# Kernel tuning notes

Hardware: AMD Instinct MI355X
Metric: run time of the kernel (lower is better)

## Reference

```python
import jax, jax.numpy as jnp
import numpy as np

ALPHA = 0.1          # LeakyReLU negative slope
NEG = -9.0e15        # mask fill value (matches torch source)
S_OUT = 64           # source_out_features
T_OUT = 64           # target_out_features


def setup_inputs() -> dict:
    key = jax.random.key(0)
    ks = jax.random.split(key, 8)
    n_s, n_t = 8192, 4096
    s_in, t_in = 128, 128
    hs = jax.random.normal(ks[0], (n_s, s_in), dtype=jnp.float32)
    ht = jax.random.normal(ks[1], (n_t, t_in), dtype=jnp.float32)
    A_opt = jax.random.randint(ks[2], (n_t, n_s), 0, 2, dtype=jnp.int32)
    # xavier_uniform with gain=1.414
    def xavier(k, shape, gain=1.414):
        fan_in, fan_out = shape[0], shape[1]
        bound = gain * np.sqrt(6.0 / (fan_in + fan_out))
        return jax.random.uniform(k, shape, jnp.float32, -bound, bound)
    Ws = xavier(ks[3], (s_in, T_OUT))
    Wt = xavier(ks[4], (t_in, S_OUT))
    a1 = xavier(ks[5], (S_OUT + T_OUT, 1))
    bias_s = jnp.zeros((T_OUT,), jnp.float32)
    bias_t = jnp.zeros((S_OUT,), jnp.float32)
    return {"hs": hs, "ht": ht, "A_opt": A_opt, "Ws": Ws, "Wt": Wt,
            "a1": a1, "bias_s": bias_s, "bias_t": bias_t}


def reference(hs, ht, A_opt, Ws, Wt, a1, bias_s, bias_t):
    # Asymmetric HOAN, eval mode (dropout=0), concatenate=True.
    Whs = hs @ Ws                       # [n_s, t_out]
    Wht = ht @ Wt                       # [n_t, s_out]
    # a1 split: first S_OUT rows pair with Wht, remaining T_OUT rows with Whs
    a_t = a1[:S_OUT, :]                 # [s_out, 1]
    a_s = a1[S_OUT:, :]                 # [t_out, 1]
    Whst = Whs @ a_s                    # [n_s, 1]
    Whtt = Wht @ a_t                    # [n_t, 1]
    e_st = jax.nn.leaky_relu(Whtt + Whst.T, ALPHA)   # [n_t, n_s]
    e_ts = jax.nn.leaky_relu(Whst + Whtt.T, ALPHA)   # [n_s, n_t]
    mask = A_opt > 0                    # [n_t, n_s]
    att_st = jax.nn.softmax(jnp.where(mask, e_st, NEG), axis=1)
    h_prime_st = att_st @ Whs + bias_s  # [n_t, t_out]
    att_ts = jax.nn.softmax(jnp.where(mask.T, e_ts, NEG), axis=1)
    h_prime_ts = att_ts @ Wht + bias_t  # [n_s, s_out]
    return jax.nn.elu(h_prime_st), jax.nn.elu(h_prime_ts)
```

## Files before the change

### kernel.cpp

```cpp
#include <hip/hip_runtime.h>
#include <math.h>

#define N_S 8192
#define N_T 4096
#define DIN 128
#define NF  64
#define SPL0 8
#define SPL1 4

typedef __attribute__((ext_vector_type(8))) short short8;
typedef __attribute__((ext_vector_type(4))) float f32x4;
typedef __attribute__((ext_vector_type(4))) int i32x4;
typedef unsigned long long u64;
typedef unsigned int u32;

__device__ __forceinline__ unsigned short f2bf(float x){
  unsigned u = __float_as_uint(x);
  unsigned r = (u + 0x7fffu + ((u >> 16) & 1u)) >> 16;
  return (unsigned short)r;
}

__device__ __forceinline__ size_t xt2_idx(int f, int k){
  return ((size_t)(k >> 5))*2048 + (size_t)((f >> 4)*512 + ((k >> 3) & 3)*128 + (f & 15)*8 + (k & 7));
}

__global__ __launch_bounds__(256) void k1_fused(
    const int* __restrict__ A,
    u64* __restrict__ RBt,
    const float* __restrict__ hs, const float* __restrict__ ht,
    const float* __restrict__ Ws, const float* __restrict__ Wt,
    const float* __restrict__ a1,
    unsigned short* __restrict__ XT2s, unsigned short* __restrict__ XT2t,
    float* __restrict__ EFs, float* __restrict__ EFt)
{
  __shared__ __align__(16) float smem[DIN*NF + 4*DIN];
  int bx = blockIdx.x;
  int t = threadIdx.x;
  if (bx < 2048) {
    u64* rbS = (u64*)smem;
    int w = t >> 6, l = t & 63;
    int i = 2*bx + (w >> 1);
    int h = w & 1;
    const int* base = A + (size_t)i*N_S + h*4096;
    #pragma unroll
    for (int it = 0; it < 16; ++it) {
      i32x4 v = *(const i32x4*)(base + it*256 + 4*l);
      u32 nib = (v.x > 0 ? 1u : 0u) | (v.y > 0 ? 2u : 0u)
              | (v.z > 0 ? 4u : 0u) | (v.w > 0 ? 8u : 0u);
      u32 b8  = nib | (((u32)__shfl_xor((int)nib, 1, 64)) << 4);
      u32 b16 = b8  | (((u32)__shfl_xor((int)b8,  2, 64)) << 8);
      u32 b32 = b16 | (((u32)__shfl_xor((int)b16, 4, 64)) << 16);
      u32 hi  = (u32)__shfl_xor((int)b32, 8, 64);
      if ((l & 15) == 0)
        rbS[(size_t)(w>>1)*128 + h*64 + it*4 + (l>>4)] = (u64)b32 | ((u64)hi << 32);
    }
    __syncthreads();
    int wi = t >> 1, ri = t & 1;
    RBt[(size_t)wi*N_T + 2*bx + ri] = rbS[(size_t)ri*128 + wi];
  } else {
    int b = bx - 2048;
    float* Wl = smem;
    float* hrow = smem + DIN*NF;
    bool is_s = b < (N_S/4);
    const float* h; const float* W; const float* av;
    unsigned short* XT; float* EFd; int r0;
    if (is_s) { r0 = b*4;           h = hs; W = Ws; av = a1 + 64; XT = XT2s; EFd = EFs; }
    else      { r0 = (b - N_S/4)*4; h = ht; W = Wt; av = a1;      XT = XT2t; EFd = EFt; }
    for (int i = t; i < DIN*NF; i += 256) Wl[i] = W[i];
    for (int i = t; i < 4*DIN;  i += 256) hrow[i] = h[(size_t)r0*DIN + i];
    __syncthreads();
    int f = t & 63, sr = t >> 6;
    float acc = 0.f;
    #pragma unroll 8
    for (int k = 0; k < DIN; ++k) acc += hrow[sr*DIN + k] * Wl[k*NF + f];
    int r = r0 + sr;
    XT[xt2_idx(f, r)] = f2bf(acc);
    float p = acc * av[f];
    #pragma unroll
    for (int o = 32; o > 0; o >>= 1) p += __shfl_xor(p, o, 64);
    if (f == 0) { EFd[2*r] = __expf(p); EFd[2*r + 1] = __expf(0.1f*p); }
  }
}

template<int DIR>
__device__ __forceinline__ void agg_body(
    int rb, int split,
    const u64* __restrict__ RBt,
    const float* __restrict__ EFu, const float* __restrict__ EFk,
    const unsigned short* __restrict__ XT2,
    float* __restrict__ accP,
    float* __restrict__ sumP,
    u64* cbS)
{
  constexpr int NK = (DIR == 0) ? N_S : N_T;
  constexpr int NU = (DIR == 0) ? N_T : N_S;
  constexpr int SPL = (DIR == 0) ? SPL0 : SPL1;
  constexpr int KCH = NK / SPL;
  int t = threadIdx.x;
  int wave = t >> 6, l = t & 63;
  int row16 = l & 15, grp = l >> 4;
  int u = rb*64 + wave*16 + row16;
  int kc0 = split * KCH;

  if (DIR == 1) {
    const u64 MM[6] = {0x00000000FFFFFFFFull, 0x0000FFFF0000FFFFull, 0x00FF00FF00FF00FFull,
                       0x0F0F0F0F0F0F0F0Full, 0x3333333333333333ull, 0x5555555555555555ull};
    const int DD[6] = {32, 16, 8, 4, 2, 1};
    #pragma unroll
    for (int cc = 0; cc < 4; ++cc) {
      int c = wave*4 + cc;
      u64 x = RBt[(size_t)rb*N_T + kc0 + c*64 + l];
      #pragma unroll
      for (int s = 0; s < 6; ++s) {
        int d = DD[s]; u64 M = MM[s];
        u32 ylo = (u32)__shfl_xor((int)(u32)x, d, 64);
        u32 yhi = (u32)__shfl_xor((int)(u32)(x >> 32), d, 64);
        u64 y = (u64)ylo | ((u64)yhi << 32);
        x = ((l & d) == 0) ? ((x & M) | ((y & M) << d))
                           : ((x & ~M) | ((y & ~M) >> d));
      }
      cbS[c*64 + l] = x;
    }
    __syncthreads();
  }

  float2 ef = *(const float2*)&EFu[2*u];
  float Eu = ef.x, Fu = ef.y;
  f32x4 acc[4];
  #pragma unroll
  for (int q = 0; q < 4; ++q) { acc[q][0]=0.f; acc[q][1]=0.f; acc[q][2]=0.f; acc[q][3]=0.f; }
  f32x4 accs; accs[0]=0.f; accs[1]=0.f; accs[2]=0.f; accs[3]=0.f;
  short8 bones;
  #pragma unroll
  for (int j = 0; j < 8; ++j) bones[j] = (short)0x3F80;

  #pragma unroll 2
  for (int k0 = kc0; k0 < kc0 + KCH; k0 += 64) {
    u64 mb = (DIR == 0) ? RBt[(size_t)(k0 >> 6)*NU + u]
                        : cbS[((k0 - kc0) >> 6)*64 + wave*16 + row16];
    u32 mlo = (u32)mb, mhi = (u32)(mb >> 32);
    short8 af01[2];
    #pragma unroll
    for (int h = 0; h < 2; ++h) {
      int kb = k0 + 32*h + grp*8;
      float4 p0 = *(const float4*)&EFk[2*kb];
      float4 p1 = *(const float4*)&EFk[2*kb + 4];
      float4 p2 = *(const float4*)&EFk[2*kb + 8];
      float4 p3 = *(const float4*)&EFk[2*kb + 12];
      float wv[8];
      wv[0] = fmaxf(Eu*p0.x, Fu*p0.y); wv[1] = fmaxf(Eu*p0.z, Fu*p0.w);
      wv[2] = fmaxf(Eu*p1.x, Fu*p1.y); wv[3] = fmaxf(Eu*p1.z, Fu*p1.w);
      wv[4] = fmaxf(Eu*p2.x, Fu*p2.y); wv[5] = fmaxf(Eu*p2.z, Fu*p2.w);
      wv[6] = fmaxf(Eu*p3.x, Fu*p3.y); wv[7] = fmaxf(Eu*p3.z, Fu*p3.w);
      u32 bb = ((h ? mhi : mlo) >> (grp*8)) & 0xffu;
      union { u32 uu[4]; short8 v; } pk;
      #pragma unroll
      for (int p = 0; p < 4; ++p) {
        int j = 2*p;
        int slo = ((int)(bb << (31 - j))) >> 31;
        int shi = ((int)(bb << (30 - j))) >> 31;
        u32 msk = __builtin_amdgcn_perm((u32)shi, (u32)slo, 0x05040100u);
        u32 w01 = __builtin_amdgcn_perm(__float_as_uint(wv[j+1]),
                                        __float_as_uint(wv[j]), 0x07060302u);
        pk.uu[p] = w01 & msk;
      }
      af01[h] = pk.v;
    }
    const unsigned short* xb = XT2 + ((size_t)(k0 >> 5))*2048 + l*8;
    #pragma unroll
    for (int q = 0; q < 4; ++q) {
      short8 b0 = *(const short8*)(xb + q*512);
      short8 b1 = *(const short8*)(xb + 2048 + q*512);
      acc[q] = __builtin_amdgcn_mfma_f32_16x16x32_bf16(af01[0], b0, acc[q], 0, 0, 0);
      acc[q] = __builtin_amdgcn_mfma_f32_16x16x32_bf16(af01[1], b1, acc[q], 0, 0, 0);
    }
    accs = __builtin_amdgcn_mfma_f32_16x16x32_bf16(af01[0], bones, accs, 0, 0, 0);
    accs = __builtin_amdgcn_mfma_f32_16x16x32_bf16(af01[1], bones, accs, 0, 0, 0);
  }

  if (row16 == 0) {
    #pragma unroll
    for (int r = 0; r < 4; ++r)
      sumP[(size_t)split*NU + rb*64 + wave*16 + grp*4 + r] = accs[r];
  }
  float* ap = accP + (size_t)split*NU*NF;
  #pragma unroll
  for (int q = 0; q < 4; ++q) {
    #pragma unroll
    for (int r = 0; r < 4; ++r) {
      int uo = rb*64 + wave*16 + grp*4 + r;
      ap[(size_t)uo*NF + q*16 + row16] = acc[q][r];
    }
  }
}

__global__ __launch_bounds__(256, 4) void agg_fused(
    const u64* __restrict__ RBt,
    const float* __restrict__ EFs, const float* __restrict__ EFt,
    const unsigned short* __restrict__ XT2s, const unsigned short* __restrict__ XT2t,
    float* __restrict__ P0, float* __restrict__ S0,
    float* __restrict__ P1, float* __restrict__ S1)
{
  __shared__ u64 cbS[16*64];
  int b = blockIdx.x;
  if (b < 64*SPL0) {
    agg_body<0>(b & 63, b >> 6, RBt, EFt, EFs, XT2s, P0, S0, cbS);
  } else {
    int b2 = b - 64*SPL0;
    agg_body<1>(b2 & 127, b2 >> 7, RBt, EFs, EFt, XT2t, P1, S1, cbS);
  }
}

__global__ __launch_bounds__(256) void finalize_kernel(
    const float* __restrict__ P0, const float* __restrict__ S0,
    const float* __restrict__ P1, const float* __restrict__ S1,
    const float* __restrict__ bias_s, const float* __restrict__ bias_t,
    float* __restrict__ out)
{
  int tid = blockIdx.x*256 + threadIdx.x;
  const int n0 = N_T*NF/4;
  float4 a = make_float4(0.f, 0.f, 0.f, 0.f);
  float den = 0.f;
  float4 bias;
  if (tid < n0) {
    int u = tid >> 4, fq = (tid & 15)*4;
    #pragma unroll
    for (int s = 0; s < SPL0; ++s) {
      float4 p = *(const float4*)&P0[((size_t)s*N_T + u)*NF + fq];
      a.x += p.x; a.y += p.y; a.z += p.z; a.w += p.w;
      den += S0[(size_t)s*N_T + u];
    }
    bias = *(const float4*)&bias_s[fq];
  } else {
    int i2 = tid - n0;
    int u = i2 >> 4, fq = (i2 & 15)*4;
    #pragma unroll
    for (int s = 0; s < SPL1; ++s) {
      float4 p = *(const float4*)&P1[((size_t)s*N_S + u)*NF + fq];
      a.x += p.x; a.y += p.y; a.z += p.z; a.w += p.w;
      den += S1[(size_t)s*N_S + u];
    }
    bias = *(const float4*)&bias_t[fq];
  }
  float inv = den > 0.f ? 1.f/den : 0.f;
  float4 v;
  v.x = a.x*inv + bias.x; v.y = a.y*inv + bias.y;
  v.z = a.z*inv + bias.z; v.w = a.w*inv + bias.w;
  v.x = v.x > 0.f ? v.x : expm1f(v.x);
  v.y = v.y > 0.f ? v.y : expm1f(v.y);
  v.z = v.z > 0.f ? v.z : expm1f(v.z);
  v.w = v.w > 0.f ? v.w : expm1f(v.w);
  *(float4*)&out[tid*4] = v;
}

extern "C" void kernel_launch(void* const* d_in, const int* in_sizes, int n_in,
                              void* d_out, int out_size, void* d_ws, size_t ws_size,
                              hipStream_t stream)
{
  const float* hs     = (const float*)d_in[0];
  const float* ht     = (const float*)d_in[1];
  const int*   A      = (const int*)  d_in[2];
  const float* Ws     = (const float*)d_in[3];
  const float* Wt     = (const float*)d_in[4];
  const float* a1     = (const float*)d_in[5];
  const float* bias_s = (const float*)d_in[6];
  const float* bias_t = (const float*)d_in[7];
  float* out = (float*)d_out;

  u64* RBt = (u64*)d_ws;
  unsigned short* XT2s = (unsigned short*)(RBt + (size_t)(N_S/64)*N_T);
  unsigned short* XT2t = XT2s + (size_t)NF*N_S;
  float* EFs = (float*)(XT2t + (size_t)NF*N_T);
  float* EFt = EFs + 2*N_S;
  float* P0  = EFt + 2*N_T;
  float* S0  = P0 + (size_t)SPL0*N_T*NF;
  float* P1  = S0 + (size_t)SPL0*N_T;
  float* S1  = P1 + (size_t)SPL1*N_S*NF;

  k1_fused<<<2048 + (N_S + N_T)/4, 256, 0, stream>>>(A, RBt, hs, ht, Ws, Wt, a1,
                                                     XT2s, XT2t, EFs, EFt);
  agg_fused<<<64*SPL0 + 128*SPL1, 256, 0, stream>>>(RBt, EFs, EFt, XT2s, XT2t,
                                                    P0, S0, P1, S1);
  finalize_kernel<<<(N_T*NF + N_S*NF)/1024, 256, 0, stream>>>(P0, S0, P1, S1,
                                                              bias_s, bias_t, out);
}
```

Measured before the change: 84.36 us.

## Compute feature projection with split-bf16 MFMA over 64-row blocks

Replaces the scalar shared-memory projection (4 rows per block, full W copied into LDS per block) with a wave-level MFMA path in which each block handles 64 rows and each wave handles 16. Inputs and weights are split into bf16 hi/lo parts and combined with three MFMAs to keep near-fp32 accuracy. The bf16 results are stored as 4-wide vectors, and the attention logit partials are reduced with shuffles. This cuts the block count and the redundant loading of W into LDS. In exchange, weights are read straight from global memory with strided scalar loads, and each element is converted on the fly.

```diff
diff --git a/kernel.cpp b/kernel.cpp
--- a/kernel.cpp
+++ b/kernel.cpp
@@ -11,6 +11,7 @@
 typedef __attribute__((ext_vector_type(8))) short short8;
 typedef __attribute__((ext_vector_type(4))) float f32x4;
 typedef __attribute__((ext_vector_type(4))) int i32x4;
+typedef __attribute__((ext_vector_type(4))) unsigned short us4;
 typedef unsigned long long u64;
 typedef unsigned int u32;
 
@@ -19,9 +20,8 @@
   unsigned r = (u + 0x7fffu + ((u >> 16) & 1u)) >> 16;
   return (unsigned short)r;
 }
-
-__device__ __forceinline__ size_t xt2_idx(int f, int k){
-  return ((size_t)(k >> 5))*2048 + (size_t)((f >> 4)*512 + ((k >> 3) & 3)*128 + (f & 15)*8 + (k & 7));
+__device__ __forceinline__ float bf2f(unsigned short s){
+  return __uint_as_float(((unsigned)s) << 16);
 }
 
 __global__ __launch_bounds__(256) void k1_fused(
@@ -33,11 +33,10 @@
     unsigned short* __restrict__ XT2s, unsigned short* __restrict__ XT2t,
     float* __restrict__ EFs, float* __restrict__ EFt)
 {
-  __shared__ __align__(16) float smem[DIN*NF + 4*DIN];
+  __shared__ u64 rbS[2*128];
   int bx = blockIdx.x;
   int t = threadIdx.x;
   if (bx < 2048) {
-    u64* rbS = (u64*)smem;
     int w = t >> 6, l = t & 63;
     int i = 2*bx + (w >> 1);
     int h = w & 1;
@@ -59,26 +58,69 @@
     RBt[(size_t)wi*N_T + 2*bx + ri] = rbS[(size_t)ri*128 + wi];
   } else {
     int b = bx - 2048;
-    float* Wl = smem;
-    float* hrow = smem + DIN*NF;
-    bool is_s = b < (N_S/4);
+    int w = t >> 6, l = t & 63, l15 = l & 15, grp = l >> 4;
+    bool is_s = b < (N_S/64);
     const float* h; const float* W; const float* av;
     unsigned short* XT; float* EFd; int r0;
-    if (is_s) { r0 = b*4;           h = hs; W = Ws; av = a1 + 64; XT = XT2s; EFd = EFs; }
-    else      { r0 = (b - N_S/4)*4; h = ht; W = Wt; av = a1;      XT = XT2t; EFd = EFt; }
-    for (int i = t; i < DIN*NF; i += 256) Wl[i] = W[i];
-    for (int i = t; i < 4*DIN;  i += 256) hrow[i] = h[(size_t)r0*DIN + i];
-    __syncthreads();
-    int f = t & 63, sr = t >> 6;
-    float acc = 0.f;
-    #pragma unroll 8
-    for (int k = 0; k < DIN; ++k) acc += hrow[sr*DIN + k] * Wl[k*NF + f];
-    int r = r0 + sr;
-    XT[xt2_idx(f, r)] = f2bf(acc);
-    float p = acc * av[f];
-    #pragma unroll
-    for (int o = 32; o > 0; o >>= 1) p += __shfl_xor(p, o, 64);
-    if (f == 0) { EFd[2*r] = __expf(p); EFd[2*r + 1] = __expf(0.1f*p); }
+    if (is_s) { r0 = b*64;              h = hs; W = Ws; av = a1 + 64; XT = XT2s; EFd = EFs; }
+    else      { r0 = (b - (N_S/64))*64; h = ht; W = Wt; av = a1;      XT = XT2t; EFd = EFt; }
+    int rbase = r0 + w*16;
+    short8 ahi[4], alo[4];
+    const float* hp0 = h + (size_t)(rbase + l15)*DIN + grp*8;
+    #pragma unroll
+    for (int kq = 0; kq < 4; ++kq) {
+      float4 x0 = *(const float4*)(hp0 + kq*32);
+      float4 x1 = *(const float4*)(hp0 + kq*32 + 4);
+      float xs[8] = {x0.x,x0.y,x0.z,x0.w,x1.x,x1.y,x1.z,x1.w};
+      #pragma unroll
+      for (int j = 0; j < 8; ++j) {
+        unsigned short hi = f2bf(xs[j]);
+        float res = xs[j] - bf2f(hi);
+        ahi[kq][j] = (short)hi; alo[kq][j] = (short)f2bf(res);
+      }
+    }
+    float part[4] = {0.f, 0.f, 0.f, 0.f};
+    #pragma unroll
+    for (int fq = 0; fq < 4; ++fq) {
+      f32x4 acc; acc[0]=0.f; acc[1]=0.f; acc[2]=0.f; acc[3]=0.f;
+      #pragma unroll
+      for (int kq = 0; kq < 4; ++kq) {
+        short8 bhi, blo;
+        #pragma unroll
+        for (int j = 0; j < 8; ++j) {
+          float x = W[(size_t)(kq*32 + grp*8 + j)*NF + fq*16 + l15];
+          unsigned short hi = f2bf(x);
+          float res = x - bf2f(hi);
+          bhi[j] = (short)hi; blo[j] = (short)f2bf(res);
+        }
+        acc = __builtin_amdgcn_mfma_f32_16x16x32_bf16(ahi[kq], bhi, acc, 0, 0, 0);
+        acc = __builtin_amdgcn_mfma_f32_16x16x32_bf16(ahi[kq], blo, acc, 0, 0, 0);
+        acc = __builtin_amdgcn_mfma_f32_16x16x32_bf16(alo[kq], bhi, acc, 0, 0, 0);
+      }
+      us4 st;
+      #pragma unroll
+      for (int r = 0; r < 4; ++r) st[r] = f2bf(acc[r]);
+      size_t basee = (size_t)((r0 >> 5) + (w >> 1))*2048 + fq*512
+                   + ((2*w + (grp >> 1)) & 3)*128 + l15*8 + (grp & 1)*4;
+      *(us4*)&XT[basee] = st;
+      float af = av[fq*16 + l15];
+      #pragma unroll
+      for (int r = 0; r < 4; ++r) part[r] += acc[r]*af;
+    }
+    #pragma unroll
+    for (int o = 1; o < 16; o <<= 1) {
+      #pragma unroll
+      for (int r = 0; r < 4; ++r) part[r] += __shfl_xor(part[r], o, 64);
+    }
+    if (l15 == 0) {
+      #pragma unroll
+      for (int r = 0; r < 4; ++r) {
+        int rr = rbase + grp*4 + r;
+        float p = part[r];
+        EFd[2*rr]     = __expf(p);
+        EFd[2*rr + 1] = __expf(0.1f*p);
+      }
+    }
   }
 }
 
@@ -277,8 +319,8 @@
   float* P1  = S0 + (size_t)SPL0*N_T;
   float* S1  = P1 + (size_t)SPL1*N_S*NF;
 
-  k1_fused<<<2048 + (N_S + N_T)/4, 256, 0, stream>>>(A, RBt, hs, ht, Ws, Wt, a1,
-                                                     XT2s, XT2t, EFs, EFt);
+  k1_fused<<<2048 + (N_S + N_T)/64, 256, 0, stream>>>(A, RBt, hs, ht, Ws, Wt, a1,
+                                                      XT2s, XT2t, EFs, EFt);
   agg_fused<<<64*SPL0 + 128*SPL1, 256, 0, stream>>>(RBt, EFs, EFt, XT2s, XT2t,
                                                     P0, S0, P1, S1);
   finalize_kernel<<<(N_T*NF + N_S*NF)/1024, 256, 0, stream>>>(P0, S0, P1, S1,
```

New measurement: 76.18 us. 9.7% less time.
